# Kernel optimization log

Hardware: AMD Instinct MI355X
Metric: run time of the kernel (lower is better)

## Reference

```python
import jax, jax.numpy as jnp
import numpy as np

DIM = 768
NUM_EXPERTS = 4
NUM_HEADS = 12
HEAD_DIM = DIM // NUM_HEADS
MLP_HID = 4 * DIM
FC1_OUT = MLP_HID + 3 * DIM   # 5376 (mlp hidden + qkv)
FC2_IN = MLP_HID + DIM        # 3840 (mlp hidden + attn out)
FC2_OUT = 2 * DIM             # 1536 (mlp out + attn proj out)
CAP_FACTOR = 0.5
LN_EPS = 1e-6


def setup_inputs() -> dict:
    key = jax.random.key(0)
    ks = jax.random.split(key, 4)
    B, N = 8, 1024
    return {
        "x": jax.random.normal(ks[0], (B, N, DIM), jnp.float32),
        "w_router": jax.random.normal(ks[1], (NUM_EXPERTS, DIM), jnp.float32) * 0.02,
        "gamma1": jnp.ones((DIM,), jnp.float32),
        "beta1": jnp.zeros((DIM,), jnp.float32),
        "w1": jax.random.normal(ks[2], (FC1_OUT, DIM), jnp.float32) * 0.02,
        "b1": jnp.zeros((FC1_OUT,), jnp.float32),
        "w2": jax.random.normal(ks[3], (FC2_OUT, FC2_IN), jnp.float32) * 0.02,
        "b2": jnp.zeros((FC2_OUT,), jnp.float32),
    }


def reference(x, w_router, gamma1, beta1, w1, b1, w2, b2):
    B, N, C = x.shape
    E = NUM_EXPERTS
    cap = int(CAP_FACTOR * N)
    # nested (MoNE) per-expert active dims: [96, 192, 384, 768] for E=4, C=768
    m = np.array([C // 2 ** (E - 1 - e) for e in range(E)])
    in_mask = (np.arange(C)[None, :] < m[:, None]).astype(np.float32)  # [E, C]
    in_mask = jnp.asarray(in_mask)
    out_mask = jnp.concatenate([in_mask, in_mask], axis=-1)  # [E, 2C] for fc2 chunks

    # ---- expert-choice router ----
    logits = jnp.einsum('bnc,ec->bne', x, w_router)          # [B, N, E]
    probs = jax.nn.softmax(logits, axis=-1)
    gate, idx = jax.lax.top_k(jnp.swapaxes(probs, 1, 2), cap)  # [B, E, cap]
    dispatch = jax.nn.one_hot(idx, N, dtype=x.dtype)           # [B, E, cap, N]
    combine = dispatch * gate[..., None]                       # [B, E, cap, N]

    # ---- norm1 ----
    mu = jnp.mean(x, -1, keepdims=True)
    var = jnp.var(x, -1, keepdims=True)
    y = (x - mu) * jax.lax.rsqrt(var + LN_EPS) * gamma1 + beta1

    # ---- experts_choose_masked_contract (fc1, nested input dims) ----
    xg = jnp.einsum('becn,bnd->becd', dispatch, y)             # gather [B,E,cap,C]
    xg = xg * in_mask[None, :, None, :]                        # nested expert slice
    h = jnp.einsum('becd,fd->becf', xg, w1) + b1               # [B,E,cap,FC1_OUT]
    h = jnp.einsum('becn,becf->bnf', dispatch, h)              # scatter [B,N,FC1_OUT]

    x_mlp, x_qkv = h[..., :MLP_HID], h[..., MLP_HID:]

    # ---- attention ----
    qkv = x_qkv.reshape(B, N, 3, NUM_HEADS, HEAD_DIM).transpose(2, 0, 3, 1, 4)
    q, k, v = qkv[0], qkv[1], qkv[2]                           # [B,H,N,hd]
    scale = HEAD_DIM ** -0.5
    attn = jax.nn.softmax(jnp.einsum('bhqd,bhkd->bhqk', q, k) * scale, axis=-1)
    x_attn = jnp.einsum('bhqk,bhkd->bhqd', attn, v)
    x_attn = x_attn.transpose(0, 2, 1, 3).reshape(B, N, C)

    # ---- mlp activation + concat ----
    x_mlp = jax.nn.gelu(x_mlp, approximate=False)
    y2 = jnp.concatenate([x_mlp, x_attn], axis=-1)             # [B,N,FC2_IN]

    # ---- experts_choose_masked_expand (fc2, nested output dims, combine-weighted) ----
    yg = jnp.einsum('becn,bnf->becf', dispatch, y2)            # gather [B,E,cap,FC2_IN]
    o = jnp.einsum('becf,of->beco', yg, w2) + b2               # [B,E,cap,FC2_OUT]
    o = o * out_mask[None, :, None, :]                         # nested expert output slice
    z = jnp.einsum('becn,beco->bno', combine, o)               # combine [B,N,FC2_OUT]

    x_mlp2, x_attn2 = z[..., :C], z[..., C:]
    return x + x_mlp2 + x_attn2
```

## Files before the change

### kernel.cpp

```cpp
#include <hip/hip_runtime.h>
#include <math.h>

typedef __bf16 bf16_t;
typedef __bf16 bf16x8 __attribute__((ext_vector_type(8)));
typedef float f32x4 __attribute__((ext_vector_type(4)));

#define DIM 768
#define NE 4
#define NH 12
#define HD 64
#define MLP_HID 3072
#define FC1_OUT 5376
#define FC2_IN 3840
#define CAP 512
#define LOG2E 1.44269504088896340736f

__device__ __forceinline__ void async_copy16(const void* g, void* l) {
  __builtin_amdgcn_global_load_lds((const __attribute__((address_space(1))) void*)g,
                                   (__attribute__((address_space(3))) void*)l, 16, 0, 0);
}

__device__ __forceinline__ float gelu_f(float v) {
  float v2 = v * v;
  float t = v * fmaf(-0.102944f, v2, -2.302208f);
  float e = exp2f(t);
  return v * __builtin_amdgcn_rcpf(1.0f + e);
}

__global__ __launch_bounds__(256) void cast_w_kernel(const float* __restrict__ w1,
                                                     const float* __restrict__ w2,
                                                     bf16_t* __restrict__ w1b,
                                                     bf16_t* __restrict__ w2b) {
  const int N1 = FC1_OUT * DIM;
  const int N2 = 1536 * FC2_IN;
  for (int i = blockIdx.x * 256 + threadIdx.x; i < N1 + N2; i += gridDim.x * 256) {
    if (i < N1) w1b[i] = (bf16_t)w1[i];
    else        w2b[i - N1] = (bf16_t)w2[i - N1];
  }
}

__global__ __launch_bounds__(256) void router_kernel(const float* __restrict__ x,
                                                     const float* __restrict__ wr,
                                                     float* __restrict__ probs) {
  int t = blockIdx.x * 4 + (threadIdx.x >> 6);
  int l = threadIdx.x & 63;
  const float* xr = x + (size_t)t * DIM;
  float a0 = 0.f, a1 = 0.f, a2 = 0.f, a3 = 0.f;
#pragma unroll
  for (int i = 0; i < 12; i++) {
    int d = l + i * 64;
    float xv = xr[d];
    a0 += xv * wr[d];
    a1 += xv * wr[DIM + d];
    a2 += xv * wr[2 * DIM + d];
    a3 += xv * wr[3 * DIM + d];
  }
#pragma unroll
  for (int off = 32; off > 0; off >>= 1) {
    a0 += __shfl_down(a0, off);
    a1 += __shfl_down(a1, off);
    a2 += __shfl_down(a2, off);
    a3 += __shfl_down(a3, off);
  }
  if (l == 0) {
    float m = fmaxf(fmaxf(a0, a1), fmaxf(a2, a3));
    float e0 = expf(a0 - m), e1 = expf(a1 - m), e2 = expf(a2 - m), e3 = expf(a3 - m);
    float inv = 1.0f / (e0 + e1 + e2 + e3);
    int b = t >> 10, n = t & 1023;
    probs[(b * NE + 0) * 1024 + n] = e0 * inv;
    probs[(b * NE + 1) * 1024 + n] = e1 * inv;
    probs[(b * NE + 2) * 1024 + n] = e2 * inv;
    probs[(b * NE + 3) * 1024 + n] = e3 * inv;
  }
}

__global__ __launch_bounds__(256) void rank_kernel(const float* __restrict__ probs,
                                                   float* __restrict__ gate_tok) {
  int be = blockIdx.y;
  __shared__ float p[1024];
  for (int i = threadIdx.x; i < 1024; i += 256) p[i] = probs[be * 1024 + i];
  __syncthreads();
  int n = blockIdx.x * 256 + threadIdx.x;
  float pn = p[n];
  int rank = 0;
  for (int j = 0; j < 1024; j++) {
    float pj = p[j];
    rank += (pj > pn) || (pj == pn && j < n);
  }
  int b = be >> 2, e = be & 3;
  gate_tok[(size_t)((b << 10) + n) * 4 + e] = (rank < CAP) ? pn : 0.0f;
}

__global__ __launch_bounds__(256) void ln_kernel(const float* __restrict__ x,
                                                 const float* __restrict__ gamma,
                                                 const float* __restrict__ beta,
                                                 const float* __restrict__ gate_tok,
                                                 bf16_t* __restrict__ ytil,
                                                 float* __restrict__ cntf,
                                                 float* __restrict__ g4) {
  int t = blockIdx.x * 4 + (threadIdx.x >> 6);
  int l = threadIdx.x & 63;
  float4 gg = ((const float4*)gate_tok)[t];
  float s0 = (gg.x > 0.f) ? 1.f : 0.f;
  float s1 = (gg.y > 0.f) ? 1.f : 0.f;
  float s2 = (gg.z > 0.f) ? 1.f : 0.f;
  float s3 = (gg.w > 0.f) ? 1.f : 0.f;
  float c3 = s3, c2 = c3 + s2, c1 = c2 + s1, c0 = c1 + s0;
  if (l == 0) {
    cntf[t] = c0;
    float4 G;
    G.x = gg.x + gg.y + gg.z + gg.w;
    G.y = gg.y + gg.z + gg.w;
    G.z = gg.z + gg.w;
    G.w = gg.w;
    ((float4*)g4)[t] = G;
  }
  const float* xr = x + (size_t)t * DIM;
  float v[12];
  float s = 0.f, sq = 0.f;
#pragma unroll
  for (int i = 0; i < 12; i++) {
    v[i] = xr[l + i * 64];
    s += v[i];
    sq += v[i] * v[i];
  }
#pragma unroll
  for (int off = 1; off < 64; off <<= 1) {
    s += __shfl_xor(s, off);
    sq += __shfl_xor(sq, off);
  }
  float mean = s * (1.0f / DIM);
  float var = sq * (1.0f / DIM) - mean * mean;
  float rs = rsqrtf(var + 1e-6f);
#pragma unroll
  for (int i = 0; i < 12; i++) {
    int d = l + i * 64;
    float cf = (d < 96) ? c0 : (d < 192) ? c1 : (d < 384) ? c2 : c3;
    ytil[(size_t)t * DIM + d] = (bf16_t)(((v[i] - mean) * rs * gamma[d] + beta[d]) * cf);
  }
}

__global__ __launch_bounds__(256, 4) void fc1_kernel(const bf16_t* __restrict__ ytil,
                                                     const bf16_t* __restrict__ w1b,
                                                     const float* __restrict__ b1,
                                                     const float* __restrict__ cntf,
                                                     bf16_t* __restrict__ y2b,
                                                     bf16_t* __restrict__ qb,
                                                     bf16_t* __restrict__ kb,
                                                     bf16_t* __restrict__ vtb) {
  const int bid = blockIdx.x;
  const int xcd = bid & 7, j = bid >> 3;
  const int mt = xcd * 8 + (j & 7);
  const int nt = j >> 3;
  const int tid = threadIdx.x;
  const int w = tid >> 6, l = tid & 63;
  const int lq = l >> 4, lr = l & 15;

  __shared__ __align__(16) bf16_t lA[128 * 64];
  __shared__ __align__(16) bf16_t lB[128 * 64];

  f32x4 acc[4][4] = {};
  const int mwave = (w & 1) * 64, nwave = (w >> 1) * 64;
  const int crow = l >> 3;
  const int cbg = (l & 7) ^ (crow & 7);

  for (int k0 = 0; k0 < DIM; k0 += 64) {
#pragma unroll
    for (int i = 0; i < 4; i++) {
      int c = w * 4 + i;
      int row = c * 8 + crow;
      async_copy16(ytil + (size_t)(mt * 128 + row) * DIM + k0 + cbg * 8, lA + c * 512);
      async_copy16(w1b + (size_t)(nt * 128 + row) * DIM + k0 + cbg * 8, lB + c * 512);
    }
    __syncthreads();
#pragma unroll
    for (int ks = 0; ks < 2; ks++) {
      const int cbA = ((ks * 4 + lq) ^ (lr & 7)) * 8;
      bf16x8 af[4], bfr[4];
#pragma unroll
      for (int mi = 0; mi < 4; mi++)
        af[mi] = *(const bf16x8*)(lA + (mwave + mi * 16 + lr) * 64 + cbA);
#pragma unroll
      for (int ni = 0; ni < 4; ni++)
        bfr[ni] = *(const bf16x8*)(lB + (nwave + ni * 16 + lr) * 64 + cbA);
#pragma unroll
      for (int mi = 0; mi < 4; mi++)
#pragma unroll
        for (int ni = 0; ni < 4; ni++)
          acc[mi][ni] = __builtin_amdgcn_mfma_f32_16x16x32_bf16(af[mi], bfr[ni], acc[mi][ni], 0, 0, 0);
    }
    __syncthreads();
  }

#pragma unroll
  for (int mi = 0; mi < 4; mi++) {
    int row0 = mt * 128 + mwave + mi * 16 + lq * 4;
    float cnt[4];
#pragma unroll
    for (int r = 0; r < 4; r++) cnt[r] = cntf[row0 + r];
#pragma unroll
    for (int ni = 0; ni < 4; ni++) {
      int col = nt * 128 + nwave + ni * 16 + lr;
      float bias = b1[col];
      if (col < MLP_HID) {
#pragma unroll
        for (int r = 0; r < 4; r++) {
          float v = acc[mi][ni][r] + cnt[r] * bias;
          y2b[(size_t)(row0 + r) * FC2_IN + col] = (bf16_t)gelu_f(v);
        }
      } else {
        int part = col - MLP_HID;
        int comp = (part >= 1536) ? 2 : (part >= 768) ? 1 : 0;
        int rem = part - comp * 768;
        int hh = rem >> 6, d = rem & 63;
#pragma unroll
        for (int r = 0; r < 4; r++) {
          float v = acc[mi][ni][r] + cnt[r] * bias;
          int t = row0 + r;
          int b = t >> 10, n = t & 1023;
          size_t base = (size_t)(b * NH + hh);
          if (comp == 0)      qb[(base * 1024 + n) * HD + d] = (bf16_t)(v * (0.125f * LOG2E));
          else if (comp == 1) kb[(base * 1024 + n) * HD + d] = (bf16_t)v;
          else                vtb[(base * HD + d) * 1024 + n] = (bf16_t)v;
        }
      }
    }
  }
}

__global__ __launch_bounds__(256) void attn_kernel(const bf16_t* __restrict__ qb,
                                                   const bf16_t* __restrict__ kb,
                                                   const bf16_t* __restrict__ vtb,
                                                   bf16_t* __restrict__ y2b) {
  const int bh = blockIdx.y;
  const int qt = blockIdx.x;
  const int tid = threadIdx.x;
  const int w = tid >> 6, l = tid & 63, lq = l >> 4, lr = l & 15;

  __shared__ __align__(16) bf16_t lK[64 * 64];
  __shared__ __align__(16) bf16_t lV[64 * 64];
  __shared__ __align__(16) bf16_t lP[4][16 * 72];

  const bf16_t* qbase = qb + (size_t)bh * 1024 * HD;
  const bf16_t* kbase = kb + (size_t)bh * 1024 * HD;
  const bf16_t* vbase = vtb + (size_t)bh * HD * 1024;

  bf16x8 qf[2];
  int qrow = qt * 64 + w * 16 + lr;
#pragma unroll
  for (int s = 0; s < 2; s++)
    qf[s] = *(const bf16x8*)(qbase + (size_t)qrow * HD + s * 32 + lq * 8);

  f32x4 oacc[4] = {};
  float psum[4] = {0.f, 0.f, 0.f, 0.f};

  const int crow = l >> 3;
  const int cbg = (l & 7) ^ (crow & 7);

  for (int kt = 0; kt < 16; kt++) {
#pragma unroll
    for (int i = 0; i < 2; i++) {
      int c = w * 2 + i;
      int row = c * 8 + crow;
      async_copy16(kbase + (size_t)(kt * 64 + row) * HD + cbg * 8, lK + c * 512);
      async_copy16(vbase + (size_t)row * 1024 + kt * 64 + cbg * 8, lV + c * 512);
    }
    __syncthreads();

    f32x4 sacc[4] = {};
#pragma unroll
    for (int s = 0; s < 2; s++) {
      const int cb = ((s * 4 + lq) ^ (lr & 7)) * 8;
#pragma unroll
      for (int kbq = 0; kbq < 4; kbq++) {
        bf16x8 kf = *(const bf16x8*)(lK + (kbq * 16 + lr) * 64 + cb);
        sacc[kbq] = __builtin_amdgcn_mfma_f32_16x16x32_bf16(qf[s], kf, sacc[kbq], 0, 0, 0);
      }
    }

#pragma unroll
    for (int kbq = 0; kbq < 4; kbq++)
#pragma unroll
      for (int r = 0; r < 4; r++) {
        float pv = exp2f(sacc[kbq][r]);
        psum[r] += pv;
        lP[w][(lq * 4 + r) * 72 + kbq * 16 + lr] = (bf16_t)pv;
      }

    bf16x8 pf[2];
#pragma unroll
    for (int s = 0; s < 2; s++)
      pf[s] = *(const bf16x8*)(&lP[w][lr * 72 + s * 32 + lq * 8]);

#pragma unroll
    for (int s = 0; s < 2; s++) {
      const int cb = ((s * 4 + lq) ^ (lr & 7)) * 8;
#pragma unroll
      for (int nb = 0; nb < 4; nb++) {
        bf16x8 vf = *(const bf16x8*)(lV + (nb * 16 + lr) * 64 + cb);
        oacc[nb] = __builtin_amdgcn_mfma_f32_16x16x32_bf16(pf[s], vf, oacc[nb], 0, 0, 0);
      }
    }
    __syncthreads();
  }

#pragma unroll
  for (int off = 1; off < 16; off <<= 1)
#pragma unroll
    for (int r = 0; r < 4; r++) psum[r] += __shfl_xor(psum[r], off);
  float rinv[4];
#pragma unroll
  for (int r = 0; r < 4; r++) rinv[r] = 1.0f / psum[r];

  int b = bh / NH, hh = bh % NH;
#pragma unroll
  for (int nb = 0; nb < 4; nb++)
#pragma unroll
    for (int r = 0; r < 4; r++) {
      float v = oacc[nb][r] * rinv[r];
      int tok = qt * 64 + w * 16 + lq * 4 + r;
      y2b[((size_t)(b * 1024 + tok)) * FC2_IN + MLP_HID + hh * HD + nb * 16 + lr] = (bf16_t)v;
    }
}

__global__ __launch_bounds__(256, 4) void fc2_kernel(const bf16_t* __restrict__ y2b,
                                                     const bf16_t* __restrict__ w2b,
                                                     const float* __restrict__ b2,
                                                     const float* __restrict__ g4,
                                                     const float* __restrict__ x,
                                                     float* __restrict__ out) {
  const int bid = blockIdx.x;
  const int xcd = bid & 7, j = bid >> 3;
  const int mt = xcd * 8 + j / 12;
  const int ct = j % 12;
  const int tid = threadIdx.x;
  const int w = tid >> 6, l = tid & 63;
  const int lq = l >> 4, lr = l & 15;

  __shared__ __align__(16) bf16_t lA[128 * 64];
  __shared__ __align__(16) bf16_t lB[128 * 64];

  f32x4 acc[2][4][2] = {};
  const int mwave = (w & 1) * 64, nwave = (w >> 1) * 32;
  const int crow = l >> 3;
  const int cbg = (l & 7) ^ (crow & 7);

  for (int k0 = 0; k0 < FC2_IN; k0 += 64) {
#pragma unroll
    for (int i = 0; i < 4; i++) {
      int c = w * 4 + i;
      int row = c * 8 + crow;
      async_copy16(y2b + (size_t)(mt * 128 + row) * FC2_IN + k0 + cbg * 8, lA + c * 512);
      int grow = ((row >> 6) * 768) + ct * 64 + (row & 63);
      async_copy16(w2b + (size_t)grow * FC2_IN + k0 + cbg * 8, lB + c * 512);
    }
    __syncthreads();
#pragma unroll
    for (int ks = 0; ks < 2; ks++) {
      const int cbA = ((ks * 4 + lq) ^ (lr & 7)) * 8;
      bf16x8 af[4], bfr[2][2];
#pragma unroll
      for (int mi = 0; mi < 4; mi++)
        af[mi] = *(const bf16x8*)(lA + (mwave + mi * 16 + lr) * 64 + cbA);
#pragma unroll
      for (int h = 0; h < 2; h++)
#pragma unroll
        for (int ni = 0; ni < 2; ni++)
          bfr[h][ni] = *(const bf16x8*)(lB + (h * 64 + nwave + ni * 16 + lr) * 64 + cbA);
#pragma unroll
      for (int h = 0; h < 2; h++)
#pragma unroll
        for (int mi = 0; mi < 4; mi++)
#pragma unroll
          for (int ni = 0; ni < 2; ni++)
            acc[h][mi][ni] = __builtin_amdgcn_mfma_f32_16x16x32_bf16(af[mi], bfr[h][ni], acc[h][mi][ni], 0, 0, 0);
    }
    __syncthreads();
  }

#pragma unroll
  for (int mi = 0; mi < 4; mi++) {
    int row0 = mt * 128 + mwave + mi * 16 + lq * 4;
    float4 G[4];
#pragma unroll
    for (int r = 0; r < 4; r++) G[r] = ((const float4*)g4)[row0 + r];
#pragma unroll
    for (int ni = 0; ni < 2; ni++) {
      int col = ct * 64 + nwave + ni * 16 + lr;
      float b20 = b2[col], b21 = b2[768 + col];
#pragma unroll
      for (int r = 0; r < 4; r++) {
        float gw = (col < 96) ? G[r].x : (col < 192) ? G[r].y : (col < 384) ? G[r].z : G[r].w;
        float o = (acc[0][mi][ni][r] + b20) + (acc[1][mi][ni][r] + b21);
        size_t idx = (size_t)(row0 + r) * DIM + col;
        out[idx] = x[idx] + gw * o;
      }
    }
  }
}

extern "C" void kernel_launch(void* const* d_in, const int* in_sizes, int n_in,
                              void* d_out, int out_size, void* d_ws, size_t ws_size,
                              hipStream_t stream) {
  const float* x     = (const float*)d_in[0];
  const float* wr    = (const float*)d_in[1];
  const float* gamma = (const float*)d_in[2];
  const float* beta  = (const float*)d_in[3];
  const float* w1    = (const float*)d_in[4];
  const float* b1    = (const float*)d_in[5];
  const float* w2    = (const float*)d_in[6];
  const float* b2    = (const float*)d_in[7];
  float* out = (float*)d_out;

  char* ws = (char*)d_ws;
  float*  probs    = (float*)(ws + 0);
  float*  gate_tok = (float*)(ws + 131072);
  float*  cntf     = (float*)(ws + 262144);
  float*  g4       = (float*)(ws + 294912);
  bf16_t* w1b      = (bf16_t*)(ws + 425984);
  bf16_t* w2b      = (bf16_t*)(ws + 8683520);
  bf16_t* ytil     = (bf16_t*)(ws + 20480000);
  bf16_t* y2b      = (bf16_t*)(ws + 33062912);
  bf16_t* qb       = (bf16_t*)(ws + 95977472);
  bf16_t* kb       = (bf16_t*)(ws + 108560384);
  bf16_t* vtb      = (bf16_t*)(ws + 121143296);

  cast_w_kernel<<<2048, 256, 0, stream>>>(w1, w2, w1b, w2b);
  router_kernel<<<2048, 256, 0, stream>>>(x, wr, probs);
  rank_kernel<<<dim3(4, 32), 256, 0, stream>>>(probs, gate_tok);
  ln_kernel<<<2048, 256, 0, stream>>>(x, gamma, beta, gate_tok, ytil, cntf, g4);
  fc1_kernel<<<2688, 256, 0, stream>>>(ytil, w1b, b1, cntf, y2b, qb, kb, vtb);
  attn_kernel<<<dim3(16, 96), 256, 0, stream>>>(qb, kb, vtb, y2b);
  fc2_kernel<<<768, 256, 0, stream>>>(y2b, w2b, b2, g4, x, out);
}
```

Baseline: 391.0 us.

## Fuse cast and router kernels, vectorize V stores, widen attention query tiles

```diff
diff --git a/kernel.cpp b/kernel.cpp
--- a/kernel.cpp
+++ b/kernel.cpp
@@ -3,6 +3,7 @@
 
 typedef __bf16 bf16_t;
 typedef __bf16 bf16x8 __attribute__((ext_vector_type(8)));
+typedef __bf16 bf16x4 __attribute__((ext_vector_type(4)));
 typedef float f32x4 __attribute__((ext_vector_type(4)));
 
 #define DIM 768
@@ -27,22 +28,23 @@
   return v * __builtin_amdgcn_rcpf(1.0f + e);
 }
 
-__global__ __launch_bounds__(256) void cast_w_kernel(const float* __restrict__ w1,
-                                                     const float* __restrict__ w2,
-                                                     bf16_t* __restrict__ w1b,
-                                                     bf16_t* __restrict__ w2b) {
-  const int N1 = FC1_OUT * DIM;
-  const int N2 = 1536 * FC2_IN;
-  for (int i = blockIdx.x * 256 + threadIdx.x; i < N1 + N2; i += gridDim.x * 256) {
-    if (i < N1) w1b[i] = (bf16_t)w1[i];
-    else        w2b[i - N1] = (bf16_t)w2[i - N1];
-  }
-}
-
-__global__ __launch_bounds__(256) void router_kernel(const float* __restrict__ x,
-                                                     const float* __restrict__ wr,
-                                                     float* __restrict__ probs) {
-  int t = blockIdx.x * 4 + (threadIdx.x >> 6);
+__global__ __launch_bounds__(256) void cast_router_kernel(const float* __restrict__ w1,
+                                                          const float* __restrict__ w2,
+                                                          bf16_t* __restrict__ w1b,
+                                                          bf16_t* __restrict__ w2b,
+                                                          const float* __restrict__ x,
+                                                          const float* __restrict__ wr,
+                                                          float* __restrict__ probs) {
+  if (blockIdx.x < 2048) {
+    const int N1 = FC1_OUT * DIM;
+    const int N2 = 1536 * FC2_IN;
+    for (int i = blockIdx.x * 256 + threadIdx.x; i < N1 + N2; i += 2048 * 256) {
+      if (i < N1) w1b[i] = (bf16_t)w1[i];
+      else        w2b[i - N1] = (bf16_t)w2[i - N1];
+    }
+    return;
+  }
+  int t = (blockIdx.x - 2048) * 4 + (threadIdx.x >> 6);
   int l = threadIdx.x & 63;
   const float* xr = x + (size_t)t * DIM;
   float a0 = 0.f, a1 = 0.f, a2 = 0.f, a3 = 0.f;
@@ -213,15 +215,21 @@
         int comp = (part >= 1536) ? 2 : (part >= 768) ? 1 : 0;
         int rem = part - comp * 768;
         int hh = rem >> 6, d = rem & 63;
-#pragma unroll
-        for (int r = 0; r < 4; r++) {
-          float v = acc[mi][ni][r] + cnt[r] * bias;
-          int t = row0 + r;
-          int b = t >> 10, n = t & 1023;
-          size_t base = (size_t)(b * NH + hh);
-          if (comp == 0)      qb[(base * 1024 + n) * HD + d] = (bf16_t)(v * (0.125f * LOG2E));
-          else if (comp == 1) kb[(base * 1024 + n) * HD + d] = (bf16_t)v;
-          else                vtb[(base * HD + d) * 1024 + n] = (bf16_t)v;
+        int b = row0 >> 10, n0 = row0 & 1023;
+        size_t base = (size_t)(b * NH + hh);
+        if (comp == 2) {
+          bf16x4 pk;
+#pragma unroll
+          for (int r = 0; r < 4; r++)
+            pk[r] = (bf16_t)(acc[mi][ni][r] + cnt[r] * bias);
+          *(bf16x4*)(vtb + (base * HD + d) * 1024 + n0) = pk;
+        } else {
+#pragma unroll
+          for (int r = 0; r < 4; r++) {
+            float v = acc[mi][ni][r] + cnt[r] * bias;
+            if (comp == 0) qb[(base * 1024 + n0 + r) * HD + d] = (bf16_t)(v * (0.125f * LOG2E));
+            else           kb[(base * 1024 + n0 + r) * HD + d] = (bf16_t)v;
+          }
         }
       }
     }
@@ -232,8 +240,10 @@
                                                    const bf16_t* __restrict__ kb,
                                                    const bf16_t* __restrict__ vtb,
                                                    bf16_t* __restrict__ y2b) {
-  const int bh = blockIdx.y;
-  const int qt = blockIdx.x;
+  const int bid = blockIdx.x;
+  const int xcd = bid & 7, j = bid >> 3;
+  const int bh = xcd * 12 + (j >> 3);
+  const int qt = j & 7;
   const int tid = threadIdx.x;
   const int w = tid >> 6, l = tid & 63, lq = l >> 4, lr = l & 15;
 
@@ -245,14 +255,17 @@
   const bf16_t* kbase = kb + (size_t)bh * 1024 * HD;
   const bf16_t* vbase = vtb + (size_t)bh * HD * 1024;
 
-  bf16x8 qf[2];
-  int qrow = qt * 64 + w * 16 + lr;
-#pragma unroll
-  for (int s = 0; s < 2; s++)
-    qf[s] = *(const bf16x8*)(qbase + (size_t)qrow * HD + s * 32 + lq * 8);
-
-  f32x4 oacc[4] = {};
-  float psum[4] = {0.f, 0.f, 0.f, 0.f};
+  bf16x8 qf[2][2];
+#pragma unroll
+  for (int h = 0; h < 2; h++) {
+    int qrow = qt * 128 + h * 64 + w * 16 + lr;
+#pragma unroll
+    for (int s = 0; s < 2; s++)
+      qf[h][s] = *(const bf16x8*)(qbase + (size_t)qrow * HD + s * 32 + lq * 8);
+  }
+
+  f32x4 oacc[2][4] = {};
+  float psum[2][4] = {};
 
   const int crow = l >> 3;
   const int cbg = (l & 7) ^ (crow & 7);
@@ -267,60 +280,65 @@
     }
     __syncthreads();
 
-    f32x4 sacc[4] = {};
-#pragma unroll
-    for (int s = 0; s < 2; s++) {
-      const int cb = ((s * 4 + lq) ^ (lr & 7)) * 8;
-#pragma unroll
-      for (int kbq = 0; kbq < 4; kbq++) {
-        bf16x8 kf = *(const bf16x8*)(lK + (kbq * 16 + lr) * 64 + cb);
-        sacc[kbq] = __builtin_amdgcn_mfma_f32_16x16x32_bf16(qf[s], kf, sacc[kbq], 0, 0, 0);
+#pragma unroll
+    for (int h = 0; h < 2; h++) {
+      f32x4 sacc[4] = {};
+#pragma unroll
+      for (int s = 0; s < 2; s++) {
+        const int cb = ((s * 4 + lq) ^ (lr & 7)) * 8;
+#pragma unroll
+        for (int kbq = 0; kbq < 4; kbq++) {
+          bf16x8 kf = *(const bf16x8*)(lK + (kbq * 16 + lr) * 64 + cb);
+          sacc[kbq] = __builtin_amdgcn_mfma_f32_16x16x32_bf16(qf[h][s], kf, sacc[kbq], 0, 0, 0);
+        }
       }
-    }
-
-#pragma unroll
-    for (int kbq = 0; kbq < 4; kbq++)
+
+#pragma unroll
+      for (int kbq = 0; kbq < 4; kbq++)
+#pragma unroll
+        for (int r = 0; r < 4; r++) {
+          float pv = exp2f(sacc[kbq][r]);
+          psum[h][r] += pv;
+          lP[w][(lq * 4 + r) * 72 + kbq * 16 + lr] = (bf16_t)pv;
+        }
+
+      bf16x8 pf[2];
+#pragma unroll
+      for (int s = 0; s < 2; s++)
+        pf[s] = *(const bf16x8*)(&lP[w][lr * 72 + s * 32 + lq * 8]);
+
+#pragma unroll
+      for (int s = 0; s < 2; s++) {
+        const int cb = ((s * 4 + lq) ^ (lr & 7)) * 8;
+#pragma unroll
+        for (int nb = 0; nb < 4; nb++) {
+          bf16x8 vf = *(const bf16x8*)(lV + (nb * 16 + lr) * 64 + cb);
+          oacc[h][nb] = __builtin_amdgcn_mfma_f32_16x16x32_bf16(pf[s], vf, oacc[h][nb], 0, 0, 0);
+        }
+      }
+    }
+    __syncthreads();
+  }
+
+  int b = bh / NH, hh = bh % NH;
+#pragma unroll
+  for (int h = 0; h < 2; h++) {
+#pragma unroll
+    for (int off = 1; off < 16; off <<= 1)
+#pragma unroll
+      for (int r = 0; r < 4; r++) psum[h][r] += __shfl_xor(psum[h][r], off);
+    float rinv[4];
+#pragma unroll
+    for (int r = 0; r < 4; r++) rinv[r] = 1.0f / psum[h][r];
+#pragma unroll
+    for (int nb = 0; nb < 4; nb++)
 #pragma unroll
       for (int r = 0; r < 4; r++) {
-        float pv = exp2f(sacc[kbq][r]);
-        psum[r] += pv;
-        lP[w][(lq * 4 + r) * 72 + kbq * 16 + lr] = (bf16_t)pv;
+        float v = oacc[h][nb][r] * rinv[r];
+        int tok = qt * 128 + h * 64 + w * 16 + lq * 4 + r;
+        y2b[((size_t)(b * 1024 + tok)) * FC2_IN + MLP_HID + hh * HD + nb * 16 + lr] = (bf16_t)v;
       }
-
-    bf16x8 pf[2];
-#pragma unroll
-    for (int s = 0; s < 2; s++)
-      pf[s] = *(const bf16x8*)(&lP[w][lr * 72 + s * 32 + lq * 8]);
-
-#pragma unroll
-    for (int s = 0; s < 2; s++) {
-      const int cb = ((s * 4 + lq) ^ (lr & 7)) * 8;
-#pragma unroll
-      for (int nb = 0; nb < 4; nb++) {
-        bf16x8 vf = *(const bf16x8*)(lV + (nb * 16 + lr) * 64 + cb);
-        oacc[nb] = __builtin_amdgcn_mfma_f32_16x16x32_bf16(pf[s], vf, oacc[nb], 0, 0, 0);
-      }
-    }
-    __syncthreads();
-  }
-
-#pragma unroll
-  for (int off = 1; off < 16; off <<= 1)
-#pragma unroll
-    for (int r = 0; r < 4; r++) psum[r] += __shfl_xor(psum[r], off);
-  float rinv[4];
-#pragma unroll
-  for (int r = 0; r < 4; r++) rinv[r] = 1.0f / psum[r];
-
-  int b = bh / NH, hh = bh % NH;
-#pragma unroll
-  for (int nb = 0; nb < 4; nb++)
-#pragma unroll
-    for (int r = 0; r < 4; r++) {
-      float v = oacc[nb][r] * rinv[r];
-      int tok = qt * 64 + w * 16 + lq * 4 + r;
-      y2b[((size_t)(b * 1024 + tok)) * FC2_IN + MLP_HID + hh * HD + nb * 16 + lr] = (bf16_t)v;
-    }
+  }
 }
 
 __global__ __launch_bounds__(256, 4) void fc2_kernel(const bf16_t* __restrict__ y2b,
@@ -425,11 +443,10 @@
   bf16_t* kb       = (bf16_t*)(ws + 108560384);
   bf16_t* vtb      = (bf16_t*)(ws + 121143296);
 
-  cast_w_kernel<<<2048, 256, 0, stream>>>(w1, w2, w1b, w2b);
-  router_kernel<<<2048, 256, 0, stream>>>(x, wr, probs);
+  cast_router_kernel<<<4096, 256, 0, stream>>>(w1, w2, w1b, w2b, x, wr, probs);
   rank_kernel<<<dim3(4, 32), 256, 0, stream>>>(probs, gate_tok);
   ln_kernel<<<2048, 256, 0, stream>>>(x, gamma, beta, gate_tok, ytil, cntf, g4);
   fc1_kernel<<<2688, 256, 0, stream>>>(ytil, w1b, b1, cntf, y2b, qb, kb, vtb);
-  attn_kernel<<<dim3(16, 96), 256, 0, stream>>>(qb, kb, vtb, y2b);
+  attn_kernel<<<768, 256, 0, stream>>>(qb, kb, vtb, y2b);
   fc2_kernel<<<768, 256, 0, stream>>>(y2b, w2b, b2, g4, x, out);
 }
```

After: 379.6 us. 1.03x faster.
